# Optimization experiments

Hardware: AMD Instinct MI355X
Metric: run time of the kernel (lower is better)

Reference implementation:

```python
import jax, jax.numpy as jnp
import numpy as np

N_TOKENS = 16384
D_MODEL = 2048
N_EXPERTS = 64
TOP_K = 8
TAU = 1.0
HYSTERESIS = 0.1
LAMBDA_TAX = 0.04
ALPHA_DAMPING = 0.7
SINKHORN_ITERS = 10


def setup_inputs() -> dict:
    key = jax.random.key(0)
    kx, kw, kb, kp, km = jax.random.split(key, 5)
    x = jax.random.normal(kx, (N_TOKENS, D_MODEL), dtype=jnp.float32)
    # LazyLinear(n_experts): weight [E, D], bias [E]
    W = jax.random.normal(kw, (N_EXPERTS, D_MODEL), dtype=jnp.float32) * (1.0 / np.sqrt(D_MODEL))
    b = jax.random.normal(kb, (N_EXPERTS,), dtype=jnp.float32) * 0.01
    # prev_probs buffer: a valid probability distribution per token
    prev_probs = jax.nn.softmax(jax.random.normal(kp, (N_TOKENS, N_EXPERTS), dtype=jnp.float32), axis=-1)
    # prev_mask buffer: exactly k experts active per token (what forward produces)
    scores = jax.random.normal(km, (N_TOKENS, N_EXPERTS), dtype=jnp.float32)
    idx = jax.lax.top_k(scores, TOP_K)[1]
    prev_mask = jnp.zeros((N_TOKENS, N_EXPERTS), dtype=bool).at[jnp.arange(N_TOKENS)[:, None], idx].set(True)
    return {"x": x, "W": W, "b": b, "prev_probs": prev_probs, "prev_mask": prev_mask}


def _router_probs(x, W, b, prev_probs, prev_mask):
    n = x.shape[0]
    logits = x @ W.T + b                               # [N, E]
    logits = logits - jnp.mean(logits, axis=-1, keepdims=True)
    M = jax.nn.softmax(logits / TAU, axis=-1)
    # Exact analytical gradient correction (correlation tax)
    C = M.T @ M                                        # [E, E]
    C = C * (1.0 - jnp.eye(N_EXPERTS, dtype=C.dtype))  # fill_diagonal_(0)
    grad_m = 4.0 * (M @ C)
    exact_grad = M * grad_m - M * jnp.sum(M * grad_m, axis=-1, keepdims=True)
    logits = logits - LAMBDA_TAX * exact_grad
    M = jax.nn.softmax(logits / TAU, axis=-1)
    # Convergent Sinkhorn-Knopp (10 fixed iterations)
    def body(i, M):
        M = M / jnp.clip(jnp.sum(M, axis=0, keepdims=True), 1e-12)
        M = M * (N_EXPERTS / n)
        M = M / jnp.clip(jnp.sum(M, axis=1, keepdims=True), 1e-12)
        return M
    M = jax.lax.fori_loop(0, SINKHORN_ITERS, body, M)
    # Momental damping with previous probs
    M = (1.0 - ALPHA_DAMPING) * prev_probs + ALPHA_DAMPING * M
    # Hysteresis blend with previous mask
    prev = prev_mask.astype(M.dtype)
    denom = jnp.clip(jnp.sum(prev, axis=-1, keepdims=True), 1.0)
    M = (1.0 - HYSTERESIS) * M + HYSTERESIS * (prev / denom)
    M = M / jnp.clip(jnp.sum(M, axis=-1, keepdims=True), 1e-12)
    return M


def reference(x, W, b, prev_probs, prev_mask):
    M = _router_probs(x, W, b, prev_probs, prev_mask)
    idx = jax.lax.top_k(M, TOP_K)[1]                   # [N, k]
    n = M.shape[0]
    mask = jnp.zeros(M.shape, dtype=bool).at[jnp.arange(n)[:, None], idx].set(True)
    return M, mask
```

## Files before the change

### kernel.cpp

```cpp
#include <hip/hip_runtime.h>
#include <math.h>

#define NT 16384
#define DM 2048
#define NE 64
#define TOPK 8
#define LTAX 0.04f
#define HYST 0.1f
#define ALPHA 0.7f

typedef unsigned int u32;
typedef unsigned short u16;
typedef unsigned long long u64;
typedef __attribute__((ext_vector_type(8))) short bf16x8;
typedef __attribute__((ext_vector_type(4))) float f32x4;

__device__ __forceinline__ float warp4_sum(float v) {
  v += __shfl_xor(v, 1); v += __shfl_xor(v, 2); return v;
}
__device__ __forceinline__ float warp4_max(float v) {
  v = fmaxf(v, __shfl_xor(v, 1)); v = fmaxf(v, __shfl_xor(v, 2)); return v;
}
__device__ __forceinline__ u16 f2bf(float f) {
  u32 u = __float_as_uint(f);
  return (u16)((u + 0x7fffu + ((u >> 16) & 1u)) >> 16);
}
__device__ __forceinline__ float bf2f(u16 h) { return __uint_as_float(((u32)h) << 16); }

__device__ __forceinline__ void split3(float a, short& h, short& m, short& l) {
  u16 hh = f2bf(a);  float r1 = a - bf2f(hh);
  u16 mm = f2bf(r1); float r2 = r1 - bf2f(mm);
  h = (short)hh; m = (short)mm; l = (short)f2bf(r2);
}

__device__ __forceinline__ u64 to_fx(float v) {
  return (u64)__double2ll_rn((double)v * 4294967296.0);
}

__global__ void k_init(const float* __restrict__ W, u16* __restrict__ Wh,
                       u16* __restrict__ Wm, u16* __restrict__ Wl,
                       u64* __restrict__ zp) {
  const int bid = blockIdx.x, tid = threadIdx.x;
  if (bid < 128) {
    int idx = (bid * 256 + tid) * 4;
    float4 v = *(const float4*)(W + idx);
    short h[4], m[4], l[4];
    split3(v.x, h[0], m[0], l[0]);
    split3(v.y, h[1], m[1], l[1]);
    split3(v.z, h[2], m[2], l[2]);
    split3(v.w, h[3], m[3], l[3]);
    *(ushort4*)(Wh + idx) = make_ushort4((u16)h[0], (u16)h[1], (u16)h[2], (u16)h[3]);
    *(ushort4*)(Wm + idx) = make_ushort4((u16)m[0], (u16)m[1], (u16)m[2], (u16)m[3]);
    *(ushort4*)(Wl + idx) = make_ushort4((u16)l[0], (u16)l[1], (u16)l[2], (u16)l[3]);
  } else {
    int i = (bid - 128) * 256 + tid;
    if (i < 26624) zp[i] = 0ull;
  }
}

__launch_bounds__(256, 4)
__global__ void k_gemm(const float* __restrict__ x, const u16* __restrict__ Whg,
                       const u16* __restrict__ Wmg, const u16* __restrict__ Wlg,
                       float* __restrict__ Lpart) {
  __shared__ __align__(16) u16 XS[30720];
  const int tid = threadIdx.x;
  const int bid = blockIdx.x;
  const int tile = bid >> 2, ks = bid & 3;
  const int row0 = tile * 64;
  const int k0 = ks * 512;
  const int lane = tid & 63, w = tid >> 6, l15 = lane & 15, l4 = lane >> 4;
  const int srow = tid >> 2, c8 = (tid & 3) * 8;
  const int stoff = srow * 40 + c8;

  f32x4 accA[4], accB[4];
  double accD[4][4];
#pragma unroll
  for (int eb = 0; eb < 4; eb++) {
    accA[eb] = (f32x4)0.f; accB[eb] = (f32x4)0.f;
#pragma unroll
    for (int r = 0; r < 4; r++) accD[eb][r] = 0.0;
  }

  float4 xq0, xq1;
  uint4 whv, wmv, wlv;
  const float* xrowp = x + (size_t)(row0 + srow) * DM + k0 + c8;
  const u16* whp = Whg + srow * DM + k0 + c8;
  const u16* wmp = Wmg + srow * DM + k0 + c8;
  const u16* wlp = Wlg + srow * DM + k0 + c8;

#define LOADCH(KC) { \
    xq0 = *(const float4*)(xrowp + (KC)); \
    xq1 = *(const float4*)(xrowp + (KC) + 4); \
    whv = *(const uint4*)(whp + (KC)); \
    wmv = *(const uint4*)(wmp + (KC)); \
    wlv = *(const uint4*)(wlp + (KC)); }

#define WRITECH(B) { \
    short ha[8], ma[8], la[8]; \
    split3(xq0.x, ha[0], ma[0], la[0]); \
    split3(xq0.y, ha[1], ma[1], la[1]); \
    split3(xq0.z, ha[2], ma[2], la[2]); \
    split3(xq0.w, ha[3], ma[3], la[3]); \
    split3(xq1.x, ha[4], ma[4], la[4]); \
    split3(xq1.y, ha[5], ma[5], la[5]); \
    split3(xq1.z, ha[6], ma[6], la[6]); \
    split3(xq1.w, ha[7], ma[7], la[7]); \
    bf16x8 xh8, xm8, xl8; \
    _Pragma("unroll") \
    for (int z = 0; z < 8; z++) { xh8[z] = ha[z]; xm8[z] = ma[z]; xl8[z] = la[z]; } \
    *(bf16x8*)(XS + 0     + (B) * 2560 + stoff) = xh8; \
    *(bf16x8*)(XS + 5120  + (B) * 2560 + stoff) = xm8; \
    *(bf16x8*)(XS + 10240 + (B) * 2560 + stoff) = xl8; \
    *(uint4*)(XS + 15360 + (B) * 2560 + stoff) = whv; \
    *(uint4*)(XS + 20480 + (B) * 2560 + stoff) = wmv; \
    *(uint4*)(XS + 25600 + (B) * 2560 + stoff) = wlv; }

#define COMPUTECH(B) { \
    const int ar = (w * 16 + l15) * 40 + l4 * 8; \
    bf16x8 ah = *(const bf16x8*)(XS + 0     + (B) * 2560 + ar); \
    bf16x8 am = *(const bf16x8*)(XS + 5120  + (B) * 2560 + ar); \
    bf16x8 al = *(const bf16x8*)(XS + 10240 + (B) * 2560 + ar); \
    _Pragma("unroll") \
    for (int eb = 0; eb < 4; eb++) { \
      const int br = (eb * 16 + l15) * 40 + l4 * 8; \
      bf16x8 bh = *(const bf16x8*)(XS + 15360 + (B) * 2560 + br); \
      bf16x8 bm = *(const bf16x8*)(XS + 20480 + (B) * 2560 + br); \
      bf16x8 bl = *(const bf16x8*)(XS + 25600 + (B) * 2560 + br); \
      accA[eb] = __builtin_amdgcn_mfma_f32_16x16x32_bf16(ah, bh, accA[eb], 0, 0, 0); \
      accB[eb] = __builtin_amdgcn_mfma_f32_16x16x32_bf16(ah, bm, accB[eb], 0, 0, 0); \
      accB[eb] = __builtin_amdgcn_mfma_f32_16x16x32_bf16(am, bh, accB[eb], 0, 0, 0); \
      accB[eb] = __builtin_amdgcn_mfma_f32_16x16x32_bf16(am, bm, accB[eb], 0, 0, 0); \
      accB[eb] = __builtin_amdgcn_mfma_f32_16x16x32_bf16(ah, bl, accB[eb], 0, 0, 0); \
      accB[eb] = __builtin_amdgcn_mfma_f32_16x16x32_bf16(al, bh, accB[eb], 0, 0, 0); \
    } }

  LOADCH(0);
  WRITECH(0);
  __syncthreads();
#pragma unroll 1
  for (int t = 0; t < 16; t++) {
    if (t < 15) LOADCH((t + 1) * 32);
    COMPUTECH(t & 1);
    if ((t & 7) == 7) {
#pragma unroll
      for (int eb = 0; eb < 4; eb++) {
#pragma unroll
        for (int r = 0; r < 4; r++)
          accD[eb][r] += (double)accA[eb][r] + (double)accB[eb][r];
        accA[eb] = (f32x4)0.f; accB[eb] = (f32x4)0.f;
      }
    }
    if (t < 15) WRITECH((t + 1) & 1);
    __syncthreads();
  }

  float* outp = Lpart + (size_t)ks * NT * NE;
#pragma unroll
  for (int eb = 0; eb < 4; eb++)
#pragma unroll
    for (int r = 0; r < 4; r++) {
      int trow = w * 16 + l4 * 4 + r;
      outp[(size_t)(row0 + trow) * NE + eb * 16 + l15] = (float)accD[eb][r];
    }
}

__launch_bounds__(256)
__global__ void k_post(const float* __restrict__ Lpart, const float* __restrict__ b,
                       float* __restrict__ Lbuf, u64* __restrict__ CmAcc) {
  __shared__ float ms[64 * 68];
  const int tid = threadIdx.x, bid = blockIdx.x;
  const int tg = tid >> 2, q = tid & 3;
  const int row = bid * 64 + tg;
  float l[16], m[16];
  {
    double acc[16];
#pragma unroll
    for (int j = 0; j < 16; j++) acc[j] = 0.0;
#pragma unroll 1
    for (int ks = 0; ks < 4; ks++) {
      const float* p = Lpart + (size_t)ks * NT * NE + (size_t)row * NE + q * 16;
#pragma unroll
      for (int i = 0; i < 4; i++) {
        float4 v = *(const float4*)(p + i * 4);
        acc[i * 4 + 0] += (double)v.x; acc[i * 4 + 1] += (double)v.y;
        acc[i * 4 + 2] += (double)v.z; acc[i * 4 + 3] += (double)v.w;
      }
    }
#pragma unroll
    for (int i = 0; i < 4; i++) {
      float4 bv = *(const float4*)(b + q * 16 + i * 4);
      l[i * 4 + 0] = (float)acc[i * 4 + 0] + bv.x;
      l[i * 4 + 1] = (float)acc[i * 4 + 1] + bv.y;
      l[i * 4 + 2] = (float)acc[i * 4 + 2] + bv.z;
      l[i * 4 + 3] = (float)acc[i * 4 + 3] + bv.w;
    }
    float s = 0.f;
#pragma unroll
    for (int j = 0; j < 16; j++) s += l[j];
    s = warp4_sum(s);
    const float mean = s * (1.0f / 64.0f);
    float mx = -1e30f;
#pragma unroll
    for (int j = 0; j < 16; j++) { l[j] -= mean; mx = fmaxf(mx, l[j]); }
    mx = warp4_max(mx);
#pragma unroll
    for (int i = 0; i < 4; i++)
      *(float4*)(Lbuf + (size_t)row * NE + q * 16 + i * 4) =
          make_float4(l[i * 4], l[i * 4 + 1], l[i * 4 + 2], l[i * 4 + 3]);
    float ps = 0.f;
#pragma unroll
    for (int j = 0; j < 16; j++) { m[j] = expf(l[j] - mx); ps += m[j]; }
    ps = warp4_sum(ps);
    const float inv = 1.0f / ps;
#pragma unroll
    for (int j = 0; j < 16; j++) m[j] *= inv;
#pragma unroll
    for (int i = 0; i < 4; i++)
      *(float4*)(ms + tg * 68 + q * 16 + i * 4) =
          make_float4(m[i * 4], m[i * 4 + 1], m[i * 4 + 2], m[i * 4 + 3]);
  }
  __syncthreads();
  const int gi0 = (tid >> 4) * 4;
  const int gj0 = (tid & 15) * 4;
  float ga[4][4];
#pragma unroll
  for (int a = 0; a < 4; a++)
#pragma unroll
    for (int c = 0; c < 4; c++) ga[a][c] = 0.f;
  for (int t = 0; t < 64; t++) {
    float4 a = *(const float4*)(ms + t * 68 + gi0);
    float4 bb = *(const float4*)(ms + t * 68 + gj0);
    ga[0][0] = fmaf(a.x, bb.x, ga[0][0]); ga[0][1] = fmaf(a.x, bb.y, ga[0][1]);
    ga[0][2] = fmaf(a.x, bb.z, ga[0][2]); ga[0][3] = fmaf(a.x, bb.w, ga[0][3]);
    ga[1][0] = fmaf(a.y, bb.x, ga[1][0]); ga[1][1] = fmaf(a.y, bb.y, ga[1][1]);
    ga[1][2] = fmaf(a.y, bb.z, ga[1][2]); ga[1][3] = fmaf(a.y, bb.w, ga[1][3]);
    ga[2][0] = fmaf(a.z, bb.x, ga[2][0]); ga[2][1] = fmaf(a.z, bb.y, ga[2][1]);
    ga[2][2] = fmaf(a.z, bb.z, ga[2][2]); ga[2][3] = fmaf(a.z, bb.w, ga[2][3]);
    ga[3][0] = fmaf(a.w, bb.x, ga[3][0]); ga[3][1] = fmaf(a.w, bb.y, ga[3][1]);
    ga[3][2] = fmaf(a.w, bb.z, ga[3][2]); ga[3][3] = fmaf(a.w, bb.w, ga[3][3]);
  }
  u64* slot = CmAcc + (size_t)(bid & 3) * 4096;
#pragma unroll
  for (int ii = 0; ii < 4; ii++)
#pragma unroll
    for (int jj = 0; jj < 4; jj++)
      atomicAdd(slot + (gi0 + ii) * 64 + gj0 + jj, to_fx(ga[ii][jj]));
}

__launch_bounds__(256)
__global__ void k_correct(const float* __restrict__ Lbuf, const u64* __restrict__ CmAcc,
                          float* __restrict__ M0, u64* __restrict__ p0Acc) {
  __shared__ float ms[64 * 68];
  __shared__ float Cs[4096];
  __shared__ float cred[256];
  const int tid = threadIdx.x, bid = blockIdx.x;
  const int tg = tid >> 2, q = tid & 3;
  const int lane = tid & 63, w = tid >> 6;
  const int row = bid * 64 + tg;
  float l[16], m[16];
#pragma unroll
  for (int i = 0; i < 4; i++) {
    float4 lv = *(const float4*)(Lbuf + (size_t)row * NE + q * 16 + i * 4);
    l[i * 4 + 0] = lv.x; l[i * 4 + 1] = lv.y; l[i * 4 + 2] = lv.z; l[i * 4 + 3] = lv.w;
  }
  {
    float mx = -1e30f;
#pragma unroll
    for (int j = 0; j < 16; j++) mx = fmaxf(mx, l[j]);
    mx = warp4_max(mx);
    float ps = 0.f;
#pragma unroll
    for (int j = 0; j < 16; j++) { m[j] = expf(l[j] - mx); ps += m[j]; }
    ps = warp4_sum(ps);
    const float inv = 1.0f / ps;
#pragma unroll
    for (int j = 0; j < 16; j++) m[j] *= inv;
#pragma unroll
    for (int i = 0; i < 4; i++)
      *(float4*)(ms + tg * 68 + q * 16 + i * 4) =
          make_float4(m[i * 4], m[i * 4 + 1], m[i * 4 + 2], m[i * 4 + 3]);
  }
#pragma unroll 4
  for (int i = 0; i < 16; i++) {
    int idx = tid + i * 256;
    u64 s = CmAcc[idx] + CmAcc[4096 + idx] + CmAcc[8192 + idx] + CmAcc[12288 + idx];
    float v = (float)((double)s * (1.0 / 4294967296.0));
    int r = idx >> 6, c = idx & 63;
    Cs[idx] = (r == c) ? 0.f : v;
  }
  __syncthreads();
  {
    float g[16];
#pragma unroll
    for (int j = 0; j < 16; j++) g[j] = 0.f;
    for (int f = 0; f < 64; f++) {
      float mf = ms[tg * 68 + f];
#pragma unroll
      for (int i = 0; i < 4; i++) {
        float4 cv = *(const float4*)(Cs + f * 64 + q * 16 + i * 4);
        g[i * 4 + 0] = fmaf(mf, cv.x, g[i * 4 + 0]);
        g[i * 4 + 1] = fmaf(mf, cv.y, g[i * 4 + 1]);
        g[i * 4 + 2] = fmaf(mf, cv.z, g[i * 4 + 2]);
        g[i * 4 + 3] = fmaf(mf, cv.w, g[i * 4 + 3]);
      }
    }
    float dot = 0.f;
#pragma unroll
    for (int j = 0; j < 16; j++) { g[j] *= 4.f; dot += m[j] * g[j]; }
    dot = warp4_sum(dot);
    float mx = -1e30f;
#pragma unroll
    for (int j = 0; j < 16; j++) {
      l[j] = l[j] - LTAX * (m[j] * (g[j] - dot));
      mx = fmaxf(mx, l[j]);
    }
    mx = warp4_max(mx);
    float ps = 0.f;
#pragma unroll
    for (int j = 0; j < 16; j++) { m[j] = expf(l[j] - mx); ps += m[j]; }
    ps = warp4_sum(ps);
    const float inv = 1.0f / ps;
#pragma unroll
    for (int j = 0; j < 16; j++) m[j] *= inv;
#pragma unroll
    for (int i = 0; i < 4; i++)
      *(float4*)(M0 + (size_t)row * NE + q * 16 + i * 4) =
          make_float4(m[i * 4], m[i * 4 + 1], m[i * 4 + 2], m[i * 4 + 3]);
  }
  {
    float cs[16];
#pragma unroll
    for (int j = 0; j < 16; j++) cs[j] = m[j];
#pragma unroll
    for (int j = 0; j < 16; j++) {
      cs[j] += __shfl_xor(cs[j], 4);  cs[j] += __shfl_xor(cs[j], 8);
      cs[j] += __shfl_xor(cs[j], 16); cs[j] += __shfl_xor(cs[j], 32);
    }
    if ((lane >> 2) == 0) {
#pragma unroll
      for (int j = 0; j < 16; j++) cred[w * 64 + lane * 16 + j] = cs[j];
    }
    __syncthreads();
    if (tid < 64)
      atomicAdd(p0Acc + (size_t)(bid & 15) * 64 + tid,
                to_fx(cred[tid] + cred[64 + tid] + cred[128 + tid] + cred[192 + tid]));
  }
}

__launch_bounds__(256)
__global__ void k_sink(const float* __restrict__ M0, const u64* __restrict__ pin,
                       u64* __restrict__ pout) {
  __shared__ u64 pred[4][64];
  __shared__ float fac[64];
  __shared__ float cred[256];
  const int tid = threadIdx.x, bid = blockIdx.x;
  const int tg = tid >> 2, q = tid & 3;
  const int lane = tid & 63, w = tid >> 6;
  const int row = bid * 64 + tg;
  {
    const int grp = tid >> 6, e = tid & 63;
    pred[grp][e] = pin[grp * 64 + e] + pin[(grp + 4) * 64 + e] +
                   pin[(grp + 8) * 64 + e] + pin[(grp + 12) * 64 + e];
  }
  __syncthreads();
  if (tid < 64) {
    u64 s = pred[0][tid] + pred[1][tid] + pred[2][tid] + pred[3][tid];
    float P = (float)((double)s * (1.0 / 4294967296.0));
    fac[tid] = 256.0f / fmaxf(P, 1e-30f);
  }
  __syncthreads();
  float mv[16];
#pragma unroll
  for (int i = 0; i < 4; i++) {
    float4 v = *(const float4*)(M0 + (size_t)row * NE + q * 16 + i * 4);
    mv[i * 4 + 0] = v.x; mv[i * 4 + 1] = v.y; mv[i * 4 + 2] = v.z; mv[i * 4 + 3] = v.w;
  }
  float Q = 0.f;
#pragma unroll
  for (int j = 0; j < 16; j++) Q = fmaf(mv[j], fac[q * 16 + j], Q);
  Q = warp4_sum(Q);
  const float U = 1.0f / fmaxf(Q, 1e-30f);
  float cs[16];
#pragma unroll
  for (int j = 0; j < 16; j++) cs[j] = U * mv[j];
#pragma unroll
  for (int j = 0; j < 16; j++) {
    cs[j] += __shfl_xor(cs[j], 4);  cs[j] += __shfl_xor(cs[j], 8);
    cs[j] += __shfl_xor(cs[j], 16); cs[j] += __shfl_xor(cs[j], 32);
  }
  if ((lane >> 2) == 0) {
#pragma unroll
    for (int j = 0; j < 16; j++) cred[w * 64 + lane * 16 + j] = cs[j];
  }
  __syncthreads();
  if (tid < 64)
    atomicAdd(pout + (size_t)(bid & 15) * 64 + tid,
              to_fx(cred[tid] + cred[64 + tid] + cred[128 + tid] + cred[192 + tid]));
}

__launch_bounds__(256)
__global__ void k_final(const float* __restrict__ M0, const u64* __restrict__ pin,
                        const float* __restrict__ pp, const void* __restrict__ pmask,
                        float* __restrict__ out) {
  __shared__ u64 pred[4][64];
  __shared__ float fac[64];
  __shared__ int s_cnt[256];
  __shared__ int s_flag;
  const int tid = threadIdx.x, bid = blockIdx.x;
  const int tg = tid >> 2, q = tid & 3;
  const int lane = tid & 63;
  const int row = bid * 64 + tg;

  {
    uint4 v = ((const uint4*)pmask)[tid];
    int c = 0; u32 ww;
    ww = v.x; c += ((ww & 0xffu) != 0) + ((ww & 0xff00u) != 0) + ((ww & 0xff0000u) != 0) + ((ww & 0xff000000u) != 0);
    ww = v.y; c += ((ww & 0xffu) != 0) + ((ww & 0xff00u) != 0) + ((ww & 0xff0000u) != 0) + ((ww & 0xff000000u) != 0);
    ww = v.z; c += ((ww & 0xffu) != 0) + ((ww & 0xff00u) != 0) + ((ww & 0xff0000u) != 0) + ((ww & 0xff000000u) != 0);
    ww = v.w; c += ((ww & 0xffu) != 0) + ((ww & 0xff00u) != 0) + ((ww & 0xff0000u) != 0) + ((ww & 0xff000000u) != 0);
    s_cnt[tid] = c;
    __syncthreads();
    for (int s = 128; s; s >>= 1) { if (tid < s) s_cnt[tid] += s_cnt[tid + s]; __syncthreads(); }
    if (tid == 0) { int n = s_cnt[0]; s_flag = (n > 384) ? 0 : ((n > 192) ? 2 : 1); }
  }
  {
    const int grp = tid >> 6, e = tid & 63;
    pred[grp][e] = pin[grp * 64 + e] + pin[(grp + 4) * 64 + e] +
                   pin[(grp + 8) * 64 + e] + pin[(grp + 12) * 64 + e];
  }
  __syncthreads();
  if (tid < 64) {
    u64 s = pred[0][tid] + pred[1][tid] + pred[2][tid] + pred[3][tid];
    float P = (float)((double)s * (1.0 / 4294967296.0));
    fac[tid] = 256.0f / fmaxf(P, 1e-30f);
  }
  __syncthreads();

  float mv[16];
#pragma unroll
  for (int i = 0; i < 4; i++) {
    float4 v = *(const float4*)(M0 + (size_t)row * NE + q * 16 + i * 4);
    mv[i * 4 + 0] = v.x; mv[i * 4 + 1] = v.y; mv[i * 4 + 2] = v.z; mv[i * 4 + 3] = v.w;
  }
  float Q = 0.f;
#pragma unroll
  for (int j = 0; j < 16; j++) Q = fmaf(mv[j], fac[q * 16 + j], Q);
  Q = warp4_sum(Q);
  const float U = 1.0f / fmaxf(Q, 1e-30f);
  float m[16];
#pragma unroll
  for (int j = 0; j < 16; j++) m[j] = U * mv[j] * fac[q * 16 + j];

  const int flag = s_flag;
  float pv[16], mk[16];
#pragma unroll
  for (int i = 0; i < 4; i++) {
    float4 v = *(const float4*)(pp + (size_t)row * NE + q * 16 + i * 4);
    pv[i * 4 + 0] = v.x; pv[i * 4 + 1] = v.y; pv[i * 4 + 2] = v.z; pv[i * 4 + 3] = v.w;
  }
  if (flag == 0) {
    const u32* pb = (const u32*)pmask + row * 16 + q * 4;
#pragma unroll
    for (int i = 0; i < 4; i++) {
      u32 ww = pb[i];
      mk[i * 4 + 0] = (ww & 0xffu) ? 1.f : 0.f;
      mk[i * 4 + 1] = (ww & 0xff00u) ? 1.f : 0.f;
      mk[i * 4 + 2] = (ww & 0xff0000u) ? 1.f : 0.f;
      mk[i * 4 + 3] = (ww & 0xff000000u) ? 1.f : 0.f;
    }
  } else if (flag == 1) {
    const int* pb = (const int*)pmask + (size_t)row * NE + q * 16;
#pragma unroll
    for (int j = 0; j < 16; j++) mk[j] = pb[j] ? 1.f : 0.f;
  } else {
    const float* pb = (const float*)pmask + (size_t)row * NE + q * 16;
#pragma unroll
    for (int j = 0; j < 16; j++) mk[j] = (pb[j] != 0.f) ? 1.f : 0.f;
  }
  float msum = 0.f;
#pragma unroll
  for (int j = 0; j < 16; j++) msum += mk[j];
  msum = warp4_sum(msum);
  const float hscale = HYST / fmaxf(msum, 1.0f);
  float v[16];
  float s = 0.f;
#pragma unroll
  for (int j = 0; j < 16; j++) {
    float base = (1.f - ALPHA) * pv[j] + ALPHA * m[j];
    v[j] = (1.f - HYST) * base + hscale * mk[j];
    s += v[j];
  }
  s = warp4_sum(s);
  const float inv = 1.0f / fmaxf(s, 1e-12f);
#pragma unroll
  for (int j = 0; j < 16; j++) v[j] *= inv;

  float* mout = out;
  float* kout = out + (size_t)NT * NE;
#pragma unroll
  for (int i = 0; i < 4; i++)
    *(float4*)(mout + (size_t)row * NE + q * 16 + i * 4) =
        make_float4(v[i * 4], v[i * 4 + 1], v[i * 4 + 2], v[i * 4 + 3]);

  int cnt[16];
#pragma unroll
  for (int j = 0; j < 16; j++) cnt[j] = 0;
  const int base = lane & ~3;
#pragma unroll
  for (int oq = 0; oq < 4; oq++) {
#pragma unroll
    for (int j2 = 0; j2 < 16; j2++) {
      float ov = __shfl(v[j2], base + oq, 64);
      int oe = oq * 16 + j2;
#pragma unroll
      for (int j = 0; j < 16; j++) {
        int me = q * 16 + j;
        if (ov > v[j] || (ov == v[j] && oe < me)) cnt[j]++;
      }
    }
  }
#pragma unroll
  for (int i = 0; i < 4; i++)
    *(float4*)(kout + (size_t)row * NE + q * 16 + i * 4) =
        make_float4(cnt[i * 4] < TOPK ? 1.f : 0.f, cnt[i * 4 + 1] < TOPK ? 1.f : 0.f,
                    cnt[i * 4 + 2] < TOPK ? 1.f : 0.f, cnt[i * 4 + 3] < TOPK ? 1.f : 0.f);
}

extern "C" void kernel_launch(void* const* d_in, const int* in_sizes, int n_in,
                              void* d_out, int out_size, void* d_ws, size_t ws_size,
                              hipStream_t stream) {
  const float* x = (const float*)d_in[0];
  const float* W = (const float*)d_in[1];
  const float* b = (const float*)d_in[2];
  const float* pp = (const float*)d_in[3];
  const void* pmask = d_in[4];
  float* out = (float*)d_out;

  unsigned char* wsb = (unsigned char*)d_ws;
  u16* Wh = (u16*)(wsb);
  u16* Wm = (u16*)(wsb + 262144);
  u16* Wl = (u16*)(wsb + 524288);
  float* Lpart = (float*)(wsb + 786432);
  float* Lbuf = (float*)(wsb + 17563648);
  float* M0buf = (float*)(wsb + 21757952);
  u64* CmAcc = (u64*)(wsb + 25952256);
  u64* pAcc = (u64*)(wsb + 26083328);

  k_init<<<232, 256, 0, stream>>>(W, Wh, Wm, Wl, CmAcc);
  k_gemm<<<1024, 256, 0, stream>>>(x, Wh, Wm, Wl, Lpart);
  k_post<<<256, 256, 0, stream>>>(Lpart, b, Lbuf, CmAcc);
  k_correct<<<256, 256, 0, stream>>>(Lbuf, CmAcc, M0buf, pAcc);
  for (int k = 1; k <= 9; k++)
    k_sink<<<256, 256, 0, stream>>>(M0buf, pAcc + (size_t)(k - 1) * 1024,
                                    pAcc + (size_t)k * 1024);
  k_final<<<256, 256, 0, stream>>>(M0buf, pAcc + (size_t)9 * 1024, pp, pmask, out);
}
```

Before: 180.1 us.

## Split GEMM K dimension eight ways with single-buffered LDS and more blocks

The split-K factor of the router GEMM goes from 4 to 8, doubling the grid to 2048 blocks. LDS is halved by dropping the double buffer, and occupancy is raised to 5 blocks per CU. The double-precision periodic accumulation is replaced by a single float-to-double sum at the end. The cost is a load-sync-write-sync-compute loop with no overlap between global loads and MFMA, twice the partial-logit traffic (8 slices of 4 MB) read back in k_post, and a larger workspace.

```diff
diff --git a/kernel.cpp b/kernel.cpp
--- a/kernel.cpp
+++ b/kernel.cpp
@@ -58,28 +58,23 @@
   }
 }
 
-__launch_bounds__(256, 4)
+__launch_bounds__(256, 5)
 __global__ void k_gemm(const float* __restrict__ x, const u16* __restrict__ Whg,
                        const u16* __restrict__ Wmg, const u16* __restrict__ Wlg,
                        float* __restrict__ Lpart) {
-  __shared__ __align__(16) u16 XS[30720];
+  __shared__ __align__(16) u16 XS[15360];
   const int tid = threadIdx.x;
   const int bid = blockIdx.x;
-  const int tile = bid >> 2, ks = bid & 3;
+  const int tile = bid >> 3, ks = bid & 7;
   const int row0 = tile * 64;
-  const int k0 = ks * 512;
+  const int k0 = ks * 256;
   const int lane = tid & 63, w = tid >> 6, l15 = lane & 15, l4 = lane >> 4;
   const int srow = tid >> 2, c8 = (tid & 3) * 8;
   const int stoff = srow * 40 + c8;
 
   f32x4 accA[4], accB[4];
-  double accD[4][4];
-#pragma unroll
-  for (int eb = 0; eb < 4; eb++) {
-    accA[eb] = (f32x4)0.f; accB[eb] = (f32x4)0.f;
-#pragma unroll
-    for (int r = 0; r < 4; r++) accD[eb][r] = 0.0;
-  }
+#pragma unroll
+  for (int eb = 0; eb < 4; eb++) { accA[eb] = (f32x4)0.f; accB[eb] = (f32x4)0.f; }
 
   float4 xq0, xq1;
   uint4 whv, wmv, wlv;
@@ -95,7 +90,7 @@
     wmv = *(const uint4*)(wmp + (KC)); \
     wlv = *(const uint4*)(wlp + (KC)); }
 
-#define WRITECH(B) { \
+#define WRITECH() { \
     short ha[8], ma[8], la[8]; \
     split3(xq0.x, ha[0], ma[0], la[0]); \
     split3(xq0.y, ha[1], ma[1], la[1]); \
@@ -108,24 +103,24 @@
     bf16x8 xh8, xm8, xl8; \
     _Pragma("unroll") \
     for (int z = 0; z < 8; z++) { xh8[z] = ha[z]; xm8[z] = ma[z]; xl8[z] = la[z]; } \
-    *(bf16x8*)(XS + 0     + (B) * 2560 + stoff) = xh8; \
-    *(bf16x8*)(XS + 5120  + (B) * 2560 + stoff) = xm8; \
-    *(bf16x8*)(XS + 10240 + (B) * 2560 + stoff) = xl8; \
-    *(uint4*)(XS + 15360 + (B) * 2560 + stoff) = whv; \
-    *(uint4*)(XS + 20480 + (B) * 2560 + stoff) = wmv; \
-    *(uint4*)(XS + 25600 + (B) * 2560 + stoff) = wlv; }
-
-#define COMPUTECH(B) { \
+    *(bf16x8*)(XS + 0     + stoff) = xh8; \
+    *(bf16x8*)(XS + 2560  + stoff) = xm8; \
+    *(bf16x8*)(XS + 5120  + stoff) = xl8; \
+    *(uint4*)(XS + 7680  + stoff) = whv; \
+    *(uint4*)(XS + 10240 + stoff) = wmv; \
+    *(uint4*)(XS + 12800 + stoff) = wlv; }
+
+#define COMPUTECH() { \
     const int ar = (w * 16 + l15) * 40 + l4 * 8; \
-    bf16x8 ah = *(const bf16x8*)(XS + 0     + (B) * 2560 + ar); \
-    bf16x8 am = *(const bf16x8*)(XS + 5120  + (B) * 2560 + ar); \
-    bf16x8 al = *(const bf16x8*)(XS + 10240 + (B) * 2560 + ar); \
+    bf16x8 ah = *(const bf16x8*)(XS + 0    + ar); \
+    bf16x8 am = *(const bf16x8*)(XS + 2560 + ar); \
+    bf16x8 al = *(const bf16x8*)(XS + 5120 + ar); \
     _Pragma("unroll") \
     for (int eb = 0; eb < 4; eb++) { \
       const int br = (eb * 16 + l15) * 40 + l4 * 8; \
-      bf16x8 bh = *(const bf16x8*)(XS + 15360 + (B) * 2560 + br); \
-      bf16x8 bm = *(const bf16x8*)(XS + 20480 + (B) * 2560 + br); \
-      bf16x8 bl = *(const bf16x8*)(XS + 25600 + (B) * 2560 + br); \
+      bf16x8 bh = *(const bf16x8*)(XS + 7680  + br); \
+      bf16x8 bm = *(const bf16x8*)(XS + 10240 + br); \
+      bf16x8 bl = *(const bf16x8*)(XS + 12800 + br); \
       accA[eb] = __builtin_amdgcn_mfma_f32_16x16x32_bf16(ah, bh, accA[eb], 0, 0, 0); \
       accB[eb] = __builtin_amdgcn_mfma_f32_16x16x32_bf16(ah, bm, accB[eb], 0, 0, 0); \
       accB[eb] = __builtin_amdgcn_mfma_f32_16x16x32_bf16(am, bh, accB[eb], 0, 0, 0); \
@@ -134,24 +129,13 @@
       accB[eb] = __builtin_amdgcn_mfma_f32_16x16x32_bf16(al, bh, accB[eb], 0, 0, 0); \
     } }
 
-  LOADCH(0);
-  WRITECH(0);
-  __syncthreads();
 #pragma unroll 1
-  for (int t = 0; t < 16; t++) {
-    if (t < 15) LOADCH((t + 1) * 32);
-    COMPUTECH(t & 1);
-    if ((t & 7) == 7) {
-#pragma unroll
-      for (int eb = 0; eb < 4; eb++) {
-#pragma unroll
-        for (int r = 0; r < 4; r++)
-          accD[eb][r] += (double)accA[eb][r] + (double)accB[eb][r];
-        accA[eb] = (f32x4)0.f; accB[eb] = (f32x4)0.f;
-      }
-    }
-    if (t < 15) WRITECH((t + 1) & 1);
+  for (int t = 0; t < 8; t++) {
+    LOADCH(t * 32);
     __syncthreads();
+    WRITECH();
+    __syncthreads();
+    COMPUTECH();
   }
 
   float* outp = Lpart + (size_t)ks * NT * NE;
@@ -160,7 +144,8 @@
 #pragma unroll
     for (int r = 0; r < 4; r++) {
       int trow = w * 16 + l4 * 4 + r;
-      outp[(size_t)(row0 + trow) * NE + eb * 16 + l15] = (float)accD[eb][r];
+      outp[(size_t)(row0 + trow) * NE + eb * 16 + l15] =
+          (float)((double)accA[eb][r] + (double)accB[eb][r]);
     }
 }
 
@@ -177,7 +162,7 @@
 #pragma unroll
     for (int j = 0; j < 16; j++) acc[j] = 0.0;
 #pragma unroll 1
-    for (int ks = 0; ks < 4; ks++) {
+    for (int ks = 0; ks < 8; ks++) {
       const float* p = Lpart + (size_t)ks * NT * NE + (size_t)row * NE + q * 16;
 #pragma unroll
       for (int i = 0; i < 4; i++) {
@@ -541,13 +526,13 @@
   u16* Wm = (u16*)(wsb + 262144);
   u16* Wl = (u16*)(wsb + 524288);
   float* Lpart = (float*)(wsb + 786432);
-  float* Lbuf = (float*)(wsb + 17563648);
-  float* M0buf = (float*)(wsb + 21757952);
-  u64* CmAcc = (u64*)(wsb + 25952256);
-  u64* pAcc = (u64*)(wsb + 26083328);
+  float* Lbuf = (float*)(wsb + 34340864);
+  float* M0buf = (float*)(wsb + 38535168);
+  u64* CmAcc = (u64*)(wsb + 42729472);
+  u64* pAcc = (u64*)(wsb + 42860544);
 
   k_init<<<232, 256, 0, stream>>>(W, Wh, Wm, Wl, CmAcc);
-  k_gemm<<<1024, 256, 0, stream>>>(x, Wh, Wm, Wl, Lpart);
+  k_gemm<<<2048, 256, 0, stream>>>(x, Wh, Wm, Wl, Lpart);
   k_post<<<256, 256, 0, stream>>>(Lpart, b, Lbuf, CmAcc);
   k_correct<<<256, 256, 0, stream>>>(Lbuf, CmAcc, M0buf, pAcc);
   for (int k = 1; k <= 9; k++)
```

Result: faster. 176.4 us (-2.0%).
